# Kernel tuning notes

Hardware: AMD Instinct MI355X
Metric: run time of the kernel (lower is better)

## Reference

```python
import jax, jax.numpy as jnp
import numpy as np

EPS = 1e-5  # torch BatchNorm1d default eps
O, T, D, H1, H2 = 8, 4, 256, 64, 32


def setup_inputs() -> dict:
    key = jax.random.key(0)
    ks = jax.random.split(key, 8)
    B = 65536
    feature = jax.random.normal(ks[0], (B, D), dtype=jnp.float32)
    treatment = jax.random.randint(ks[1], (B,), 0, T, dtype=jnp.int64)
    s1 = 1.0 / np.sqrt(D)
    s2 = 1.0 / np.sqrt(H1)
    s3 = 1.0 / np.sqrt(H2)
    params = {
        # per (outcome, treatment) expert MLP weights
        'W1': jax.random.uniform(ks[2], (O, T, D, H1), jnp.float32, -s1, s1),
        'b1': jnp.zeros((O, T, H1), jnp.float32),
        'g1': jnp.ones((O, T, H1), jnp.float32),   # BN1 gamma
        'be1': jnp.zeros((O, T, H1), jnp.float32),  # BN1 beta
        'm1': jnp.zeros((O, T, H1), jnp.float32),   # BN1 running mean
        'v1': jnp.ones((O, T, H1), jnp.float32),    # BN1 running var
        'W2': jax.random.uniform(ks[3], (O, T, H1, H2), jnp.float32, -s2, s2),
        'b2': jnp.zeros((O, T, H2), jnp.float32),
        'g2': jnp.ones((O, T, H2), jnp.float32),
        'be2': jnp.zeros((O, T, H2), jnp.float32),
        'm2': jnp.zeros((O, T, H2), jnp.float32),
        'v2': jnp.ones((O, T, H2), jnp.float32),
        'W3': jax.random.uniform(ks[4], (O, T, H2), jnp.float32, -s3, s3),  # final Linear(32,1), squeezed
        'b3': jnp.zeros((O, T), jnp.float32),
    }
    return {'feature': feature, 'treatment': treatment, **params}


def _tlearner_fwd(x, t, W1, b1, g1, be1, m1, v1, W2, b2, g2, be2, m2, v2, W3, b3):
    # Dense evaluation of every (outcome, treatment) expert, then per-row
    # selection by treatment id. Equivalent (in eval mode: BN uses running
    # stats, dropout off) to the masked dispatch of the original module.
    h = jnp.einsum('bd,otdh->both', x, W1) + b1          # [B,O,T,H1]
    h = jax.nn.relu(h)
    h = (h - m1) * jax.lax.rsqrt(v1 + EPS) * g1 + be1    # BN1 (eval)
    h = jnp.einsum('both,othk->botk', h, W2) + b2        # [B,O,T,H2]
    h = jax.nn.relu(h)
    h = (h - m2) * jax.lax.rsqrt(v2 + EPS) * g2 + be2    # BN2 (eval)
    out = jnp.einsum('botk,otk->bot', h, W3) + b3        # [B,O,T]
    idx = t.astype(jnp.int32)[:, None, None]             # [B,1,1]
    return jnp.take_along_axis(out, jnp.broadcast_to(idx, (out.shape[0], O, 1)), axis=2)[..., 0]  # [B,O]


def reference(feature, treatment, W1, b1, g1, be1, m1, v1, W2, b2, g2, be2, m2, v2, W3, b3):
    return _tlearner_fwd(feature, treatment, W1, b1, g1, be1, m1, v1,
                         W2, b2, g2, be2, m2, v2, W3, b3)
```

## Files before the change

### kernel.cpp

```cpp
#include <hip/hip_runtime.h>
#include <cstdint>

typedef short bf16x8 __attribute__((ext_vector_type(8)));
typedef float f32x4 __attribute__((ext_vector_type(4)));

#define NO 8
#define NT 4
#define ND 256
#define NH1 64
#define NH2 32
#define BM 32
#define BNEPS 1e-5f

#define GLD(srcp, dstp) __builtin_amdgcn_global_load_lds( \
    (const __attribute__((address_space(1))) void*)(srcp), \
    (__attribute__((address_space(3))) void*)(dstp), 16, 0, 0)

__device__ __forceinline__ unsigned bfpack2(float a, float b) {
    unsigned ua = __float_as_uint(a), ub = __float_as_uint(b);
    ua = (ua + 0x7FFFu + ((ua >> 16) & 1u)) >> 16;
    ub = (ub + 0x7FFFu + ((ub >> 16) & 1u)) >> 16;
    return ua | (ub << 16);
}

__device__ __forceinline__ unsigned cvtpk(float lo, float hi) {
    unsigned r;
    asm("v_cvt_pk_bf16_f32 %0, %1, %2" : "=v"(r) : "v"(lo), "v"(hi));
    return r;
}


__global__ void k_hist_prep(const int* __restrict__ trt, int* __restrict__ ws, int B,
                            const float* __restrict__ W1, const float* __restrict__ W2,
                            const float* __restrict__ b1, const float* __restrict__ g1,
                            const float* __restrict__ be1, const float* __restrict__ m1,
                            const float* __restrict__ v1,
                            const float* __restrict__ b2, const float* __restrict__ g2,
                            const float* __restrict__ be2, const float* __restrict__ m2,
                            const float* __restrict__ v2, const float* __restrict__ W3,
                            unsigned* __restrict__ W1T4, unsigned* __restrict__ W2T4,
                            float* __restrict__ P1, float* __restrict__ P2) {
    const int bid = blockIdx.x, tid = threadIdx.x;
    if (bid < 256) {
        __shared__ int loc[NT];
        if (tid < NT) loc[tid] = 0;
        __syncthreads();
        const int i = bid * 256 + tid;
        if (i < B) atomicAdd(&loc[trt[i] & 3], 1);
        __syncthreads();
        if (tid < NT) atomicAdd(&ws[tid], loc[tid]);
    } else if (bid < 512) {
        const int gi = (bid - 256) * 256 + tid;
        const int lane = gi & 63, nt = (gi >> 6) & 31, c = (gi >> 11) & 7, t = gi >> 14;
        const int n16 = lane & 15, kg = lane >> 4;
        const int n = nt * 16 + n16, o = n >> 6, h = n & 63;
        const int k0 = c * 32 + kg * 8;
        const float* src = W1 + ((size_t)(o * NT + t) * ND + k0) * NH1 + h;
        float v[8];
#pragma unroll
        for (int j = 0; j < 8; ++j) v[j] = src[(size_t)j * NH1];
        uint4 q;
        q.x = bfpack2(v[0], v[1]); q.y = bfpack2(v[2], v[3]);
        q.z = bfpack2(v[4], v[5]); q.w = bfpack2(v[6], v[7]);
        ((uint4*)W1T4)[gi] = q;
    } else if (bid < 544) {
        const int gi = (bid - 512) * 256 + tid;
        const int m16 = gi & 15, kg = (gi >> 4) & 3, ks = (gi >> 6) & 1,
                  kt = (gi >> 7) & 1, o = (gi >> 8) & 7, t = gi >> 11;
        const int k2 = kt * 16 + m16, hb = ks * 32 + kg * 8;
        const float* src = W2 + ((size_t)(o * NT + t) * NH1 + hb) * NH2 + k2;
        float v[8];
#pragma unroll
        for (int j = 0; j < 8; ++j) v[j] = src[(size_t)j * NH2];
        uint4 q;
        q.x = bfpack2(v[0], v[1]); q.y = bfpack2(v[2], v[3]);
        q.z = bfpack2(v[4], v[5]); q.w = bfpack2(v[6], v[7]);
        ((uint4*)W2T4)[gi] = q;
    } else if (bid < 552) {
        const int gi = (bid - 544) * 256 + tid;
        const int t = gi >> 9, n = gi & 511;
        const int o = n >> 6, h = n & 63;
        const int idx = (o * NT + t) * NH1 + h;
        const float sc = g1[idx] * rsqrtf(v1[idx] + BNEPS);
        P1[gi] = sc;
        P1[2048 + gi] = be1[idx] - m1[idx] * sc;
        P1[4096 + gi] = b1[idx];
    } else {
        const int gi = (bid - 552) * 256 + tid;
        const int t = gi >> 8, q = gi & 255;
        const int o = q >> 5, k2 = q & 31;
        const int idx = (o * NT + t) * NH2 + k2;
        const float s = g2[idx] * rsqrtf(v2[idx] + BNEPS);
        const float w3 = W3[idx];
        P2[gi] = s * w3;
        P2[1024 + gi] = (be2[idx] - m2[idx] * s) * w3;
        P2[2048 + gi] = b2[idx];
    }
}

__global__ void k_scatter(const int* __restrict__ trt, int* __restrict__ ws,
                          int* __restrict__ rperm, int B) {
    __shared__ int loc[NT], gb[NT];
    const int tid = threadIdx.x;
    if (tid < NT) loc[tid] = 0;
    __syncthreads();
    const int i = blockIdx.x * blockDim.x + tid;
    int tt = 0, pos = 0;
    if (i < B) { tt = trt[i] & 3; pos = atomicAdd(&loc[tt], 1); }
    __syncthreads();
    if (tid < NT) {
        const int c0 = ws[0], c1 = ws[1], c2 = ws[2];
        const int q0 = (c0 + 31) & ~31, q1 = (c1 + 31) & ~31, q2 = (c2 + 31) & ~31;
        const int eb = tid == 0 ? 0 : tid == 1 ? q0 : tid == 2 ? q0 + q1 : q0 + q1 + q2;
        gb[tid] = eb + atomicAdd(&ws[4 + tid], loc[tid]);
    }
    __syncthreads();
    if (i < B) rperm[gb[tt] + pos] = i;
}

__global__ __launch_bounds__(256, 2) void k_main(
    const float* __restrict__ X, const int* __restrict__ ws, const int* __restrict__ rperm,
    const char* __restrict__ W1T, const char* __restrict__ W2T,
    const float* __restrict__ P1, const float* __restrict__ P2,
    const float* __restrict__ pb3, float* __restrict__ out)
{
    const int c0 = ws[0], c1 = ws[1], c2 = ws[2], c3 = ws[3];
    const int q0 = (c0 + 31) & ~31, q1 = (c1 + 31) & ~31, q2 = (c2 + 31) & ~31;
    const int e0 = q0, e1 = q0 + q1, e2 = e1 + q2, e3 = e2 + ((c3 + 31) & ~31);
    const int m0 = blockIdx.x * BM;
    if (m0 >= e3) return;
    const int t = (m0 >= e0) + (m0 >= e1) + (m0 >= e2);

    const int tid = threadIdx.x;
    const int w = tid >> 6;
    const int l = tid & 63;

    __shared__ __align__(16) char LDS[65536];

    const int rid_o = rperm[m0 + (l & 31)];
    const char* Xb = (const char*)X;
    const char* W1Tt = W1T + (size_t)t * 262144;
    const int ln4 = (l >> 4) * 4;

#pragma unroll
    for (int j = 0; j < 8; ++j) {
        const int r = w * 8 + j;
        const int rr = __shfl(rid_o, r);
        const size_t rowb = (size_t)(rr < 0 ? 0 : rr) * 1024;
        const unsigned soff = (unsigned)(l * 16) ^ (unsigned)((r & 7) << 4);
        GLD(Xb + rowb + soff, LDS + r * 1024 + l * 16);
    }
#pragma unroll
    for (int u = 0; u < 8; ++u) {
        const int sl = (u * 4 + w) * 1024 + l * 16;
        GLD(W1Tt + sl, LDS + 32768 + sl);
    }

    f32x4 acc[8][2];
#pragma unroll
    for (int nt = 0; nt < 8; ++nt) {
        const int n0 = (w * 8 + nt) * 16 + ln4;
        const float4 bbv = *(const float4*)(P1 + 4096 + t * 512 + n0);
        acc[nt][0] = (f32x4){bbv.x, bbv.y, bbv.z, bbv.w};
        acc[nt][1] = acc[nt][0];
    }

    __syncthreads();

    for (int c = 0; c < 8; ++c) {
        bf16x8 aA[8];
#pragma unroll
        for (int nt = 0; nt < 8; ++nt)
            aA[nt] = *(const bf16x8*)(LDS + 32768 + (w * 8 + nt) * 1024 + l * 16);
#pragma unroll
        for (int rt = 0; rt < 2; ++rt) {
            const int r = rt * 16 + (l & 15);
            const unsigned swz = (unsigned)((r & 7) << 4);
            const unsigned b0 = (unsigned)(c * 128 + (l >> 4) * 32);
            const f32x4 xlo = *(const f32x4*)(LDS + r * 1024 + (b0 ^ swz));
            const f32x4 xhi = *(const f32x4*)(LDS + r * 1024 + ((b0 + 16) ^ swz));
            uint4 u;
            u.x = cvtpk(xlo[0], xlo[1]); u.y = cvtpk(xlo[2], xlo[3]);
            u.z = cvtpk(xhi[0], xhi[1]); u.w = cvtpk(xhi[2], xhi[3]);
            const bf16x8 bX = __builtin_bit_cast(bf16x8, u);
#pragma unroll
            for (int nt = 0; nt < 8; ++nt)
                acc[nt][rt] = __builtin_amdgcn_mfma_f32_16x16x32_bf16(aA[nt], bX, acc[nt][rt], 0, 0, 0);
        }
        if (c < 7) {
            __syncthreads();
            const char* src = W1Tt + (c + 1) * 32768;
#pragma unroll
            for (int u = 0; u < 8; ++u) {
                const int sl = (u * 4 + w) * 1024 + l * 16;
                GLD(src + sl, LDS + 32768 + sl);
            }
            __syncthreads();
        }
    }
    __syncthreads();

#pragma unroll
    for (int nt = 0; nt < 8; ++nt) {
        const int n0 = (w * 8 + nt) * 16 + ln4;
        const int p = t * 512 + n0;
        const float4 scv = *(const float4*)(P1 + p);
        const float4 shv = *(const float4*)(P1 + 2048 + p);
#pragma unroll
        for (int rt = 0; rt < 2; ++rt) {
            const int r = rt * 16 + (l & 15);
            const f32x4 a = acc[nt][rt];
            const float z0 = fmaf(fmaxf(a[0], 0.f), scv.x, shv.x);
            const float z1 = fmaf(fmaxf(a[1], 0.f), scv.y, shv.y);
            const float z2 = fmaf(fmaxf(a[2], 0.f), scv.z, shv.z);
            const float z3 = fmaf(fmaxf(a[3], 0.f), scv.w, shv.w);
            uint2 pk;
            pk.x = cvtpk(z0, z1); pk.y = cvtpk(z2, z3);
            *(uint2*)(LDS + r * 1024 + (((unsigned)(n0 * 2)) ^ (unsigned)((r & 7) << 4))) = pk;
        }
    }

    bf16x8 aW[2][2][2];
#pragma unroll
    for (int oo = 0; oo < 2; ++oo) {
        const int o = w * 2 + oo;
#pragma unroll
        for (int kt = 0; kt < 2; ++kt)
#pragma unroll
            for (int ks = 0; ks < 2; ++ks)
                aW[oo][kt][ks] = *(const bf16x8*)(W2T +
                    ((((size_t)t * NO + o) * 2 + kt) * 2 + ks) * 1024 + l * 16);
    }
    f32x4 acc2[2][2][2];
#pragma unroll
    for (int oo = 0; oo < 2; ++oo)
#pragma unroll
        for (int kt = 0; kt < 2; ++kt)
#pragma unroll
            for (int rt2 = 0; rt2 < 2; ++rt2) acc2[oo][kt][rt2] = (f32x4){0.f, 0.f, 0.f, 0.f};

#pragma unroll
    for (int rt2 = 0; rt2 < 2; ++rt2) {
        const int r = rt2 * 16 + (l & 15);
        const unsigned swz = (unsigned)((r & 7) << 4);
#pragma unroll
        for (int ks = 0; ks < 2; ++ks) {
            const int nb = ks * 32 + (l >> 4) * 8;
#pragma unroll
            for (int oo = 0; oo < 2; ++oo) {
                const int n8 = (w * 2 + oo) * 64 + nb;
                const bf16x8 bH = *(const bf16x8*)(LDS + r * 1024 + (((unsigned)(n8 * 2)) ^ swz));
#pragma unroll
                for (int kt = 0; kt < 2; ++kt)
                    acc2[oo][kt][rt2] = __builtin_amdgcn_mfma_f32_16x16x32_bf16(aW[oo][kt][ks], bH, acc2[oo][kt][rt2], 0, 0, 0);
            }
        }
    }

    float p[2][2];
#pragma unroll
    for (int oo = 0; oo < 2; ++oo)
#pragma unroll
        for (int rt2 = 0; rt2 < 2; ++rt2) p[oo][rt2] = 0.f;

#pragma unroll
    for (int oo = 0; oo < 2; ++oo) {
        const int o = w * 2 + oo;
#pragma unroll
        for (int kt = 0; kt < 2; ++kt) {
            const int q = o * 32 + kt * 16 + ln4;
            const int p3 = t * 256 + q;
            const float4 A3 = *(const float4*)(P2 + p3);
            const float4 C3 = *(const float4*)(P2 + 1024 + p3);
            const float4 bb = *(const float4*)(P2 + 2048 + p3);
#pragma unroll
            for (int rt2 = 0; rt2 < 2; ++rt2) {
                const f32x4 a = acc2[oo][kt][rt2];
                float s = fmaf(fmaxf(a[0] + bb.x, 0.f), A3.x, C3.x);
                s = fmaf(fmaxf(a[1] + bb.y, 0.f), A3.y, s + C3.y);
                s = fmaf(fmaxf(a[2] + bb.z, 0.f), A3.z, s + C3.z);
                s = fmaf(fmaxf(a[3] + bb.w, 0.f), A3.w, s + C3.w);
                p[oo][rt2] += s;
            }
        }
    }
#pragma unroll
    for (int oo = 0; oo < 2; ++oo)
#pragma unroll
        for (int rt2 = 0; rt2 < 2; ++rt2) {
            float v = p[oo][rt2];
            v += __shfl_xor(v, 16);
            v += __shfl_xor(v, 32);
            p[oo][rt2] = v;
        }

    const int oo_s = l >> 5;
    const int rt2_s = (l >> 4) & 1;
    const int o_s = w * 2 + oo_s;
    const int r = rt2_s * 16 + (l & 15);
    const float v = oo_s ? (rt2_s ? p[1][1] : p[1][0]) : (rt2_s ? p[0][1] : p[0][0]);
    const int ra = __shfl(rid_o, r);
    if (ra >= 0) out[(size_t)ra * NO + o_s] = v + pb3[o_s * NT + t];
}

extern "C" void kernel_launch(void* const* d_in, const int* in_sizes, int n_in,
                              void* d_out, int out_size, void* d_ws, size_t ws_size,
                              hipStream_t stream) {
    const float* X   = (const float*)d_in[0];
    const int* trt   = (const int*)d_in[1];
    const float* W1  = (const float*)d_in[2];
    const float* b1  = (const float*)d_in[3];
    const float* g1  = (const float*)d_in[4];
    const float* be1 = (const float*)d_in[5];
    const float* m1  = (const float*)d_in[6];
    const float* v1  = (const float*)d_in[7];
    const float* W2  = (const float*)d_in[8];
    const float* b2  = (const float*)d_in[9];
    const float* g2  = (const float*)d_in[10];
    const float* be2 = (const float*)d_in[11];
    const float* m2  = (const float*)d_in[12];
    const float* v2  = (const float*)d_in[13];
    const float* W3  = (const float*)d_in[14];
    const float* b3  = (const float*)d_in[15];
    float* out = (float*)d_out;

    const int B = in_sizes[1];
    const int permCap = B + 128;
    int* wsi   = (int*)d_ws;
    int* rperm = wsi + 16;
    char* wsb  = (char*)d_ws;
    size_t off = (64 + (size_t)permCap * 4 + 15) & ~(size_t)15;
    char* W1T = wsb + off;
    char* W2T = W1T + 1048576;
    float* P1 = (float*)(W2T + 131072);
    float* P2 = P1 + 6144;

    hipMemsetAsync(wsi, 0, 64, stream);
    hipMemsetAsync(rperm, 0xFF, (size_t)permCap * 4, stream);

    k_hist_prep<<<556, 256, 0, stream>>>(trt, wsi, B, W1, W2,
                                         b1, g1, be1, m1, v1,
                                         b2, g2, be2, m2, v2, W3,
                                         (unsigned*)W1T, (unsigned*)W2T, P1, P2);
    k_scatter<<<(B + 255) / 256, 256, 0, stream>>>(trt, wsi, rperm, B);

    const int gx = (B + 128) / 32;
    k_main<<<gx, 256, 0, stream>>>(X, wsi, rperm, W1T, W2T, P1, P2, b3, out);
}
```

Baseline: 73.40 us.

## Enlarge row tile to 128 with 512 threads and double-buffered X/W1 streaming

Each block now handles 128 gathered rows with 8 waves instead of 32 rows with 4 waves. Each staged W1 chunk is therefore reused across four times as many rows, which cuts repeated weight loads. X rows and W1 chunks are streamed per K-chunk into double-buffered LDS, so the next chunk's loads overlap the current chunk's MFMAs. This replaces the old scheme of loading all X up front and serialising W1 reloads between two barriers. The cost is 128KB of LDS per block, which limits the CU to one resident block, plus coarser per-treatment padding to multiples of 128.

```diff
diff --git a/kernel.cpp b/kernel.cpp
--- a/kernel.cpp
+++ b/kernel.cpp
@@ -9,7 +9,7 @@
 #define ND 256
 #define NH1 64
 #define NH2 32
-#define BM 32
+#define BM 128
 #define BNEPS 1e-5f
 
 #define GLD(srcp, dstp) __builtin_amdgcn_global_load_lds( \
@@ -110,7 +110,7 @@
     __syncthreads();
     if (tid < NT) {
         const int c0 = ws[0], c1 = ws[1], c2 = ws[2];
-        const int q0 = (c0 + 31) & ~31, q1 = (c1 + 31) & ~31, q2 = (c2 + 31) & ~31;
+        const int q0 = (c0 + 127) & ~127, q1 = (c1 + 127) & ~127, q2 = (c2 + 127) & ~127;
         const int eb = tid == 0 ? 0 : tid == 1 ? q0 : tid == 2 ? q0 + q1 : q0 + q1 + q2;
         gb[tid] = eb + atomicAdd(&ws[4 + tid], loc[tid]);
     }
@@ -118,15 +118,15 @@
     if (i < B) rperm[gb[tt] + pos] = i;
 }
 
-__global__ __launch_bounds__(256, 2) void k_main(
+__global__ __launch_bounds__(512, 2) void k_main(
     const float* __restrict__ X, const int* __restrict__ ws, const int* __restrict__ rperm,
     const char* __restrict__ W1T, const char* __restrict__ W2T,
     const float* __restrict__ P1, const float* __restrict__ P2,
     const float* __restrict__ pb3, float* __restrict__ out)
 {
     const int c0 = ws[0], c1 = ws[1], c2 = ws[2], c3 = ws[3];
-    const int q0 = (c0 + 31) & ~31, q1 = (c1 + 31) & ~31, q2 = (c2 + 31) & ~31;
-    const int e0 = q0, e1 = q0 + q1, e2 = e1 + q2, e3 = e2 + ((c3 + 31) & ~31);
+    const int q0 = (c0 + 127) & ~127, q1 = (c1 + 127) & ~127, q2 = (c2 + 127) & ~127;
+    const int e0 = q0, e1 = q0 + q1, e2 = e1 + q2, e3 = e2 + ((c3 + 127) & ~127);
     const int m0 = blockIdx.x * BM;
     if (m0 >= e3) return;
     const int t = (m0 >= e0) + (m0 >= e1) + (m0 >= e2);
@@ -134,51 +134,84 @@
     const int tid = threadIdx.x;
     const int w = tid >> 6;
     const int l = tid & 63;
-
-    __shared__ __align__(16) char LDS[65536];
-
-    const int rid_o = rperm[m0 + (l & 31)];
+    const int ngrp = w & 3, rgrp = w >> 2;
+
+    __shared__ __align__(16) char LDS[131072];
+    char* const XB = LDS;
+    char* const WB = LDS + 32768;
+
+    const int rid_lo = rperm[m0 + l];
+    const int rid_hi = rperm[m0 + 64 + l];
+
     const char* Xb = (const char*)X;
     const char* W1Tt = W1T + (size_t)t * 262144;
     const int ln4 = (l >> 4) * 4;
 
-#pragma unroll
-    for (int j = 0; j < 8; ++j) {
-        const int r = w * 8 + j;
-        const int rr = __shfl(rid_o, r);
-        const size_t rowb = (size_t)(rr < 0 ? 0 : rr) * 1024;
-        const unsigned soff = (unsigned)(l * 16) ^ (unsigned)((r & 7) << 4);
-        GLD(Xb + rowb + soff, LDS + r * 1024 + l * 16);
-    }
-#pragma unroll
-    for (int u = 0; u < 8; ++u) {
-        const int sl = (u * 4 + w) * 1024 + l * 16;
-        GLD(W1Tt + sl, LDS + 32768 + sl);
-    }
-
-    f32x4 acc[8][2];
+    const int xrow_in = (w & 3) * 16 + (l >> 3);
+    const unsigned xsoff = (unsigned)((l & 7) * 16) ^ (unsigned)(((l >> 3) & 7) << 4);
+
+#pragma unroll
+    for (int j = 0; j < 2; ++j) {
+        const int rloc = (w >> 2) ? 64 + xrow_in + j * 8 - 64 + 64 : xrow_in + j * 8;
+    }
+    {
+#pragma unroll
+        for (int j = 0; j < 2; ++j) {
+            const int row = (w >> 2) * 64 + (w & 3) * 16 + j * 8 + (l >> 3);
+            const int rr = (w >> 2) ? __shfl(rid_hi, (w & 3) * 16 + j * 8 + (l >> 3))
+                                    : __shfl(rid_lo, (w & 3) * 16 + j * 8 + (l >> 3));
+            const size_t rowb = (size_t)(rr < 0 ? 0 : rr) * 1024;
+            GLD(Xb + rowb + 0 * 128 + xsoff, XB + row * 128 + (l & 7) * 16);
+        }
+#pragma unroll
+        for (int u = 0; u < 4; ++u) {
+            const int sl = w * 4096 + u * 1024 + l * 16;
+            GLD(W1Tt + sl, WB + sl);
+        }
+    }
+
+    f32x4 acc[8][4];
 #pragma unroll
     for (int nt = 0; nt < 8; ++nt) {
-        const int n0 = (w * 8 + nt) * 16 + ln4;
+        const int n0 = (ngrp * 8 + nt) * 16 + ln4;
         const float4 bbv = *(const float4*)(P1 + 4096 + t * 512 + n0);
         acc[nt][0] = (f32x4){bbv.x, bbv.y, bbv.z, bbv.w};
         acc[nt][1] = acc[nt][0];
-    }
-
-    __syncthreads();
-
+        acc[nt][2] = acc[nt][0];
+        acc[nt][3] = acc[nt][0];
+    }
+
+    __syncthreads();
+
+#pragma unroll
     for (int c = 0; c < 8; ++c) {
+        const int cur = c & 1, nxt = cur ^ 1;
+        if (c < 7) {
+#pragma unroll
+            for (int j = 0; j < 2; ++j) {
+                const int row = (w >> 2) * 64 + (w & 3) * 16 + j * 8 + (l >> 3);
+                const int rr = (w >> 2) ? __shfl(rid_hi, (w & 3) * 16 + j * 8 + (l >> 3))
+                                        : __shfl(rid_lo, (w & 3) * 16 + j * 8 + (l >> 3));
+                const size_t rowb = (size_t)(rr < 0 ? 0 : rr) * 1024;
+                GLD(Xb + rowb + (c + 1) * 128 + xsoff, XB + nxt * 16384 + row * 128 + (l & 7) * 16);
+            }
+#pragma unroll
+            for (int u = 0; u < 4; ++u) {
+                const int sl = w * 4096 + u * 1024 + l * 16;
+                GLD(W1Tt + (c + 1) * 32768 + sl, WB + nxt * 32768 + sl);
+            }
+        }
         bf16x8 aA[8];
 #pragma unroll
         for (int nt = 0; nt < 8; ++nt)
-            aA[nt] = *(const bf16x8*)(LDS + 32768 + (w * 8 + nt) * 1024 + l * 16);
-#pragma unroll
-        for (int rt = 0; rt < 2; ++rt) {
-            const int r = rt * 16 + (l & 15);
+            aA[nt] = *(const bf16x8*)(WB + cur * 32768 + (ngrp * 8 + nt) * 1024 + l * 16);
+#pragma unroll
+        for (int rt = 0; rt < 4; ++rt) {
+            const int r = rgrp * 64 + rt * 16 + (l & 15);
             const unsigned swz = (unsigned)((r & 7) << 4);
-            const unsigned b0 = (unsigned)(c * 128 + (l >> 4) * 32);
-            const f32x4 xlo = *(const f32x4*)(LDS + r * 1024 + (b0 ^ swz));
-            const f32x4 xhi = *(const f32x4*)(LDS + r * 1024 + ((b0 + 16) ^ swz));
+            const unsigned b0 = (unsigned)((l >> 4) * 32);
+            const f32x4 xlo = *(const f32x4*)(XB + cur * 16384 + r * 128 + (b0 ^ swz));
+            const f32x4 xhi = *(const f32x4*)(XB + cur * 16384 + r * 128 + ((b0 + 16) ^ swz));
             uint4 u;
             u.x = cvtpk(xlo[0], xlo[1]); u.y = cvtpk(xlo[2], xlo[3]);
             u.z = cvtpk(xhi[0], xhi[1]); u.w = cvtpk(xhi[2], xhi[3]);
@@ -187,28 +220,18 @@
             for (int nt = 0; nt < 8; ++nt)
                 acc[nt][rt] = __builtin_amdgcn_mfma_f32_16x16x32_bf16(aA[nt], bX, acc[nt][rt], 0, 0, 0);
         }
-        if (c < 7) {
-            __syncthreads();
-            const char* src = W1Tt + (c + 1) * 32768;
-#pragma unroll
-            for (int u = 0; u < 8; ++u) {
-                const int sl = (u * 4 + w) * 1024 + l * 16;
-                GLD(src + sl, LDS + 32768 + sl);
-            }
-            __syncthreads();
-        }
-    }
-    __syncthreads();
+        __syncthreads();
+    }
 
 #pragma unroll
     for (int nt = 0; nt < 8; ++nt) {
-        const int n0 = (w * 8 + nt) * 16 + ln4;
+        const int n0 = (ngrp * 8 + nt) * 16 + ln4;
         const int p = t * 512 + n0;
         const float4 scv = *(const float4*)(P1 + p);
         const float4 shv = *(const float4*)(P1 + 2048 + p);
 #pragma unroll
-        for (int rt = 0; rt < 2; ++rt) {
-            const int r = rt * 16 + (l & 15);
+        for (int rt = 0; rt < 4; ++rt) {
+            const int r = rgrp * 64 + rt * 16 + (l & 15);
             const f32x4 a = acc[nt][rt];
             const float z0 = fmaf(fmaxf(a[0], 0.f), scv.x, shv.x);
             const float z1 = fmaf(fmaxf(a[1], 0.f), scv.y, shv.y);
@@ -219,88 +242,76 @@
             *(uint2*)(LDS + r * 1024 + (((unsigned)(n0 * 2)) ^ (unsigned)((r & 7) << 4))) = pk;
         }
     }
-
-    bf16x8 aW[2][2][2];
-#pragma unroll
-    for (int oo = 0; oo < 2; ++oo) {
-        const int o = w * 2 + oo;
-#pragma unroll
-        for (int kt = 0; kt < 2; ++kt)
-#pragma unroll
-            for (int ks = 0; ks < 2; ++ks)
-                aW[oo][kt][ks] = *(const bf16x8*)(W2T +
-                    ((((size_t)t * NO + o) * 2 + kt) * 2 + ks) * 1024 + l * 16);
-    }
-    f32x4 acc2[2][2][2];
-#pragma unroll
-    for (int oo = 0; oo < 2; ++oo)
-#pragma unroll
-        for (int kt = 0; kt < 2; ++kt)
-#pragma unroll
-            for (int rt2 = 0; rt2 < 2; ++rt2) acc2[oo][kt][rt2] = (f32x4){0.f, 0.f, 0.f, 0.f};
-
-#pragma unroll
-    for (int rt2 = 0; rt2 < 2; ++rt2) {
+    __syncthreads();
+
+    bf16x8 aW[2][2];
+#pragma unroll
+    for (int kt = 0; kt < 2; ++kt)
+#pragma unroll
+        for (int ks = 0; ks < 2; ++ks)
+            aW[kt][ks] = *(const bf16x8*)(W2T +
+                ((((size_t)t * NO + w) * 2 + kt) * 2 + ks) * 1024 + l * 16);
+
+    f32x4 acc2[2][8];
+#pragma unroll
+    for (int kt = 0; kt < 2; ++kt)
+#pragma unroll
+        for (int rt2 = 0; rt2 < 8; ++rt2) acc2[kt][rt2] = (f32x4){0.f, 0.f, 0.f, 0.f};
+
+#pragma unroll
+    for (int rt2 = 0; rt2 < 8; ++rt2) {
         const int r = rt2 * 16 + (l & 15);
         const unsigned swz = (unsigned)((r & 7) << 4);
 #pragma unroll
         for (int ks = 0; ks < 2; ++ks) {
-            const int nb = ks * 32 + (l >> 4) * 8;
-#pragma unroll
-            for (int oo = 0; oo < 2; ++oo) {
-                const int n8 = (w * 2 + oo) * 64 + nb;
-                const bf16x8 bH = *(const bf16x8*)(LDS + r * 1024 + (((unsigned)(n8 * 2)) ^ swz));
-#pragma unroll
-                for (int kt = 0; kt < 2; ++kt)
-                    acc2[oo][kt][rt2] = __builtin_amdgcn_mfma_f32_16x16x32_bf16(aW[oo][kt][ks], bH, acc2[oo][kt][rt2], 0, 0, 0);
-            }
-        }
-    }
-
-    float p[2][2];
-#pragma unroll
-    for (int oo = 0; oo < 2; ++oo)
-#pragma unroll
-        for (int rt2 = 0; rt2 < 2; ++rt2) p[oo][rt2] = 0.f;
-
-#pragma unroll
-    for (int oo = 0; oo < 2; ++oo) {
-        const int o = w * 2 + oo;
-#pragma unroll
-        for (int kt = 0; kt < 2; ++kt) {
-            const int q = o * 32 + kt * 16 + ln4;
-            const int p3 = t * 256 + q;
-            const float4 A3 = *(const float4*)(P2 + p3);
-            const float4 C3 = *(const float4*)(P2 + 1024 + p3);
-            const float4 bb = *(const float4*)(P2 + 2048 + p3);
-#pragma unroll
-            for (int rt2 = 0; rt2 < 2; ++rt2) {
-                const f32x4 a = acc2[oo][kt][rt2];
-                float s = fmaf(fmaxf(a[0] + bb.x, 0.f), A3.x, C3.x);
-                s = fmaf(fmaxf(a[1] + bb.y, 0.f), A3.y, s + C3.y);
-                s = fmaf(fmaxf(a[2] + bb.z, 0.f), A3.z, s + C3.z);
-                s = fmaf(fmaxf(a[3] + bb.w, 0.f), A3.w, s + C3.w);
-                p[oo][rt2] += s;
-            }
-        }
-    }
-#pragma unroll
-    for (int oo = 0; oo < 2; ++oo)
-#pragma unroll
-        for (int rt2 = 0; rt2 < 2; ++rt2) {
-            float v = p[oo][rt2];
-            v += __shfl_xor(v, 16);
-            v += __shfl_xor(v, 32);
-            p[oo][rt2] = v;
-        }
-
-    const int oo_s = l >> 5;
-    const int rt2_s = (l >> 4) & 1;
-    const int o_s = w * 2 + oo_s;
-    const int r = rt2_s * 16 + (l & 15);
-    const float v = oo_s ? (rt2_s ? p[1][1] : p[1][0]) : (rt2_s ? p[0][1] : p[0][0]);
-    const int ra = __shfl(rid_o, r);
-    if (ra >= 0) out[(size_t)ra * NO + o_s] = v + pb3[o_s * NT + t];
+            const int n8 = w * 64 + ks * 32 + (l >> 4) * 8;
+            const bf16x8 bH = *(const bf16x8*)(LDS + r * 1024 + (((unsigned)(n8 * 2)) ^ swz));
+#pragma unroll
+            for (int kt = 0; kt < 2; ++kt)
+                acc2[kt][rt2] = __builtin_amdgcn_mfma_f32_16x16x32_bf16(aW[kt][ks], bH, acc2[kt][rt2], 0, 0, 0);
+        }
+    }
+
+    float pr[8];
+#pragma unroll
+    for (int rt2 = 0; rt2 < 8; ++rt2) pr[rt2] = 0.f;
+
+#pragma unroll
+    for (int kt = 0; kt < 2; ++kt) {
+        const int q3 = w * 32 + kt * 16 + ln4;
+        const int p3 = t * 256 + q3;
+        const float4 A3 = *(const float4*)(P2 + p3);
+        const float4 C3 = *(const float4*)(P2 + 1024 + p3);
+        const float4 bb = *(const float4*)(P2 + 2048 + p3);
+#pragma unroll
+        for (int rt2 = 0; rt2 < 8; ++rt2) {
+            const f32x4 a = acc2[kt][rt2];
+            float s = fmaf(fmaxf(a[0] + bb.x, 0.f), A3.x, C3.x);
+            s = fmaf(fmaxf(a[1] + bb.y, 0.f), A3.y, s + C3.y);
+            s = fmaf(fmaxf(a[2] + bb.z, 0.f), A3.z, s + C3.z);
+            s = fmaf(fmaxf(a[3] + bb.w, 0.f), A3.w, s + C3.w);
+            pr[rt2] += s;
+        }
+    }
+#pragma unroll
+    for (int rt2 = 0; rt2 < 8; ++rt2) {
+        float v = pr[rt2];
+        v += __shfl_xor(v, 16);
+        v += __shfl_xor(v, 32);
+        pr[rt2] = v;
+    }
+
+    const float b3v = pb3[w * NT + t];
+    const int g = l >> 4;
+#pragma unroll
+    for (int h = 0; h < 2; ++h) {
+        const int rt2 = g + h * 4;
+        const int r = rt2 * 16 + (l & 15);
+        const int ra = rperm[m0 + r];
+        const float v = (g == 0) ? pr[h * 4 + 0] : (g == 1) ? pr[h * 4 + 1]
+                       : (g == 2) ? pr[h * 4 + 2] : pr[h * 4 + 3];
+        if (ra >= 0) out[(size_t)ra * NO + w] = v + b3v;
+    }
 }
 
 extern "C" void kernel_launch(void* const* d_in, const int* in_sizes, int n_in,
@@ -325,7 +336,7 @@
     float* out = (float*)d_out;
 
     const int B = in_sizes[1];
-    const int permCap = B + 128;
+    const int permCap = B + 512;
     int* wsi   = (int*)d_ws;
     int* rperm = wsi + 16;
     char* wsb  = (char*)d_ws;
@@ -344,6 +355,6 @@
                                          (unsigned*)W1T, (unsigned*)W2T, P1, P2);
     k_scatter<<<(B + 255) / 256, 256, 0, stream>>>(trt, wsi, rperm, B);
 
-    const int gx = (B + 128) / 32;
-    k_main<<<gx, 256, 0, stream>>>(X, wsi, rperm, W1T, W2T, P1, P2, b3, out);
-}
+    const int gx = (B + 512) / BM;
+    k_main<<<gx, 512, 0, stream>>>(X, wsi, rperm, W1T, W2T, P1, P2, b3, out);
+}
```

New measurement: 74.76 us. About the same (+1.8%).
